# Optimization experiments

Measured on AMD Instinct MI355X. Metric: run time of the kernel, lower is better.

## Reference

```python
import jax, jax.numpy as jnp
import numpy as np

K = 3  # number of SGC propagation hops


def setup_inputs() -> dict:
    key = jax.random.key(0)
    k1, k2, k3 = jax.random.split(key, 3)
    N, E, F = 50000, 800000, 128
    x = jax.random.normal(k1, (N, F), dtype=jnp.float32)
    edge_index = jax.random.randint(k2, (2, E), 0, N, dtype=jnp.int64)
    weight = jax.random.normal(k3, (F, 1), dtype=jnp.float32) * (1.0 / np.sqrt(F))
    bias = jnp.zeros((1,), dtype=jnp.float32)
    return {"x": x, "edge_index": edge_index, "weight": weight, "bias": bias}


def reference(x, edge_index, weight, bias):
    N = x.shape[0]
    # gcn_norm: add self-loops, symmetric normalization D^-1/2 (A+I) D^-1/2
    loops = jnp.arange(N, dtype=edge_index.dtype)
    src = jnp.concatenate([edge_index[0], loops])  # message sources
    dst = jnp.concatenate([edge_index[1], loops])  # aggregation targets
    ones = jnp.ones(src.shape[0], dtype=x.dtype)
    deg = jax.ops.segment_sum(ones, dst, num_segments=N)  # [N]
    dinv = jnp.where(deg > 0, jax.lax.rsqrt(deg), 0.0)
    norm = (dinv[src] * dinv[dst])[:, None]  # [E+N, 1]
    # K hops of S @ x
    for _ in range(K):
        x = jax.ops.segment_sum(norm * x[src], dst, num_segments=N)
    out = x @ weight + bias  # [N, 1]
    return jnp.square(out)
```

## Files before the change

kernel.cpp:

```cpp
#include <hip/hip_runtime.h>

#define FEAT 128
#define NPB 98
#define SBITS 25
#define SMASK ((1u << SBITS) - 1u)
#define NSCAT 256
#define CAPB 32
#define CAPB_SHIFT 5
#define CAP2 4096
#define CAP2_SHIFT 12
#define NGEMV 256
#define TPB 256
#define LINE 32
#define NBHIST 512

__device__ __forceinline__ void astore_f(float* p, float v) {
    __hip_atomic_store(p, v, __ATOMIC_RELAXED, __HIP_MEMORY_SCOPE_AGENT);
}
__device__ __forceinline__ void astore_i(int* p, int v) {
    __hip_atomic_store(p, v, __ATOMIC_RELAXED, __HIP_MEMORY_SCOPE_AGENT);
}
__device__ __forceinline__ int aload_i(const int* p) {
    return __hip_atomic_load(p, __ATOMIC_RELAXED, __HIP_MEMORY_SCOPE_AGENT);
}

__device__ __forceinline__ void wbar(int* arr, int* flags, int b, int ep) {
    __syncthreads();
    if (threadIdx.x == 0) {
        astore_i(&arr[b], ep);
        while (aload_i(&flags[b * LINE]) < ep) __builtin_amdgcn_s_sleep(1);
    }
    __syncthreads();
}

__global__ void k1_scat_gemv(const float* __restrict__ x, const int* __restrict__ src,
                             const int* __restrict__ dst, const float* __restrict__ w,
                             int N, int E, int NB, int chunk,
                             unsigned* __restrict__ ebuf, unsigned char* __restrict__ cnt2,
                             float* __restrict__ z) {
    const int b = blockIdx.x;
    const int t = threadIdx.x;
    if (b < NSCAT) {
        __shared__ int h[NBHIST];
        for (int i = t; i < NB; i += TPB) h[i] = 0;
        __syncthreads();
        int beg = b * chunk;
        int end = min(E, beg + chunk);
        for (int e = beg + t; e < end; e += TPB) {
            int s = src[e], d = dst[e];
            int bk  = (int)((unsigned)d / NPB);
            int loc = d - bk * NPB;
            int l = atomicAdd(&h[bk], 1);
            if (l < CAPB)
                ebuf[((size_t)(bk * NSCAT + b) << CAPB_SHIFT) + l] =
                    ((unsigned)loc << SBITS) | (unsigned)s;
        }
        __syncthreads();
        for (int i = t; i < NB; i += TPB)
            cnt2[(size_t)i * NSCAT + b] = (unsigned char)min(h[i], CAPB);
    } else {
        int gb  = b - NSCAT;
        int hw  = t >> 5;
        int l32 = t & 31;
        float4 wv = ((const float4*)w)[l32];
        for (int node = gb * 8 + hw; node < N; node += NGEMV * 8) {
            float4 xv = ((const float4*)(x + (size_t)node * FEAT))[l32];
            float s = xv.x * wv.x + xv.y * wv.y + xv.z * wv.z + xv.w * wv.w;
            #pragma unroll
            for (int o = 16; o >= 1; o >>= 1) s += __shfl_xor(s, o, 64);
            if (l32 == 0) z[node] = s;
        }
    }
}

__global__ void __launch_bounds__(TPB, 2) k2_fused(
    const unsigned* __restrict__ ebuf, const unsigned char* __restrict__ cnt2,
    const float* __restrict__ z, const float* __restrict__ bias,
    unsigned* __restrict__ ebuf2,
    float* __restrict__ u0, float* __restrict__ u1, float* __restrict__ u2,
    float* __restrict__ out, int* __restrict__ arr, int* __restrict__ flags,
    int N, int NB)
{
    const int b = blockIdx.x;
    const int t = threadIdx.x;

    if (b == NB) {
        for (int ep = 1; ep <= 3; ++ep) {
            for (;;) {
                int ok = 1;
                for (int i = t; i < NB; i += TPB)
                    if (aload_i(&arr[i]) < ep) { ok = 0; break; }
                if (__syncthreads_and(ok)) break;
                __builtin_amdgcn_s_sleep(2);
            }
            for (int i = t; i < NB; i += TPB)
                astore_i(&flags[i * LINE], ep);
        }
        return;
    }

    __shared__ float uown[NPB], dinvL[NPB], acc[NPB];
    __shared__ int   degL[NPB];
    __shared__ int   pref[TPB];
    __shared__ int   cntB_s;
    const int base = b * NPB;
    const int nn   = min(NPB, N - base);

    if (t < NPB) degL[t] = 0;
    __syncthreads();
    int cnt = cnt2[(size_t)b * NSCAT + t];
    pref[t] = cnt;
    __syncthreads();
    #pragma unroll
    for (int off = 1; off < TPB; off <<= 1) {
        int v = (t >= off) ? pref[t - off] : 0;
        __syncthreads();
        pref[t] += v;
        __syncthreads();
    }
    int mypos = pref[t] - cnt;
    if (t == TPB - 1) cntB_s = min(pref[t], CAP2);
    {
        const unsigned* cell = ebuf + ((size_t)(b * NSCAT + t) << CAPB_SHIFT);
        unsigned* dst2 = ebuf2 + ((size_t)b << CAP2_SHIFT);
        #pragma unroll 4
        for (int j = 0; j < cnt; ++j) {
            unsigned p = cell[j];
            atomicAdd(&degL[p >> SBITS], 1);
            int pos = mypos + j;
            if (pos < CAP2) dst2[pos] = p;
        }
    }
    __syncthreads();
    if (t < nn) {
        float dv = 1.0f / sqrtf(1.0f + (float)degL[t]);
        dinvL[t] = dv;
        float u = dv * z[base + t];
        uown[t] = u;
        astore_f(&u0[base + t], u);
    }
    wbar(arr, flags, b, 1);

    const unsigned* dst2 = ebuf2 + ((size_t)b << CAP2_SHIFT);
    const int cntB = cntB_s;

    if (t < NPB) acc[t] = 0.0f;
    __syncthreads();
    for (int j = t; j < cntB; j += TPB) {
        unsigned p = dst2[j];
        atomicAdd(&acc[p >> SBITS], u0[p & SMASK]);
    }
    __syncthreads();
    if (t < nn) {
        float dv = dinvL[t];
        float nu = dv * dv * (acc[t] + uown[t]);
        uown[t] = nu;
        astore_f(&u1[base + t], nu);
    }
    wbar(arr, flags, b, 2);

    if (t < NPB) acc[t] = 0.0f;
    __syncthreads();
    for (int j = t; j < cntB; j += TPB) {
        unsigned p = dst2[j];
        atomicAdd(&acc[p >> SBITS], u1[p & SMASK]);
    }
    __syncthreads();
    if (t < nn) {
        float dv = dinvL[t];
        float nu = dv * dv * (acc[t] + uown[t]);
        uown[t] = nu;
        astore_f(&u2[base + t], nu);
    }
    wbar(arr, flags, b, 3);

    if (t < NPB) acc[t] = 0.0f;
    __syncthreads();
    for (int j = t; j < cntB; j += TPB) {
        unsigned p = dst2[j];
        atomicAdd(&acc[p >> SBITS], u2[p & SMASK]);
    }
    __syncthreads();
    if (t < nn) {
        float dv = dinvL[t];
        float v = dv * (acc[t] + uown[t]) + bias[0];
        out[base + t] = v * v;
    }
    if (t == 0) { astore_i(&arr[b], 0); astore_i(&flags[b * LINE], 0); }
}

__global__ void f_init_deg(float* __restrict__ deg, int N) {
    int i = blockIdx.x * blockDim.x + threadIdx.x;
    if (i < N) deg[i] = 1.0f;
}
__global__ void f_count_deg(const int* __restrict__ dst, float* __restrict__ deg, int E) {
    int e = blockIdx.x * blockDim.x + threadIdx.x;
    if (e < E) unsafeAtomicAdd(&deg[dst[e]], 1.0f);
}
__global__ void f_dot_dinv(const float* __restrict__ x, const float* __restrict__ w,
                           const float* __restrict__ deg, float* __restrict__ dinv,
                           float* __restrict__ z, int N) {
    int wid  = (blockIdx.x * blockDim.x + threadIdx.x) >> 6;
    int lane = threadIdx.x & 63;
    if (wid >= N) return;
    const float2* xr = reinterpret_cast<const float2*>(x + (size_t)wid * FEAT);
    const float2* wr = reinterpret_cast<const float2*>(w);
    float2 xv = xr[lane];
    float2 wv = wr[lane];
    float s = xv.x * wv.x + xv.y * wv.y;
    #pragma unroll
    for (int o = 32; o >= 1; o >>= 1) s += __shfl_xor(s, o, 64);
    if (lane == 0) { z[wid] = s; dinv[wid] = 1.0f / sqrtf(deg[wid]); }
}
__global__ void f_hop_self(const float* __restrict__ za, const float* __restrict__ dinv,
                           float* __restrict__ zb, int N) {
    int i = blockIdx.x * blockDim.x + threadIdx.x;
    if (i < N) { float d = dinv[i]; zb[i] = d * d * za[i]; }
}
__global__ void f_hop_edges(const int* __restrict__ src, const int* __restrict__ dst,
                            const float* __restrict__ za, const float* __restrict__ dinv,
                            float* __restrict__ zb, int E) {
    int e = blockIdx.x * blockDim.x + threadIdx.x;
    if (e < E) {
        int s = src[e], d = dst[e];
        unsafeAtomicAdd(&zb[d], dinv[s] * dinv[d] * za[s]);
    }
}
__global__ void f_final(const float* __restrict__ z, const float* __restrict__ bias,
                        float* __restrict__ out, int N) {
    int i = blockIdx.x * blockDim.x + threadIdx.x;
    if (i < N) { float v = z[i] + bias[0]; out[i] = v * v; }
}

extern "C" void kernel_launch(void* const* d_in, const int* in_sizes, int n_in,
                              void* d_out, int out_size, void* d_ws, size_t ws_size,
                              hipStream_t stream) {
    const float* x    = (const float*)d_in[0];
    const int*   ei   = (const int*)d_in[1];
    const float* w    = (const float*)d_in[2];
    const float* bias = (const float*)d_in[3];
    float*       out  = (float*)d_out;

    const int N = in_sizes[0] / FEAT;
    const int E = in_sizes[1] / 2;
    const int* src = ei;
    const int* dst = ei + E;

    const int NB = (N + NPB - 1) / NPB;

    size_t ebuf_b  = (size_t)NB * NSCAT * CAPB * sizeof(unsigned);
    size_t ebuf2_b = (size_t)NB * CAP2 * sizeof(unsigned);
    size_t off_e2    = ebuf_b;
    size_t off_z     = off_e2 + ebuf2_b;
    size_t off_arr   = (off_z + (size_t)4 * N * sizeof(float) + 255) & ~(size_t)255;
    size_t off_flags = (off_arr + (size_t)NB * sizeof(int) + 255) & ~(size_t)255;
    size_t off_cnt2  = off_flags + (size_t)NB * LINE * sizeof(int);
    size_t need      = off_cnt2 + (size_t)NB * NSCAT + 256;

    bool fast = (NB + 1 <= 512) && (N <= (1 << SBITS)) &&
                ((size_t)E <= (size_t)8 * NB * NSCAT) &&
                ((size_t)E * 2 <= (size_t)NB * CAP2) &&
                (ws_size >= need);

    if (fast) {
        unsigned*      ebuf  = (unsigned*)d_ws;
        unsigned*      ebuf2 = (unsigned*)((char*)d_ws + off_e2);
        float*         z     = (float*)((char*)d_ws + off_z);
        float*         u0    = z + N;
        float*         u1    = u0 + N;
        float*         u2    = u1 + N;
        int*           arr   = (int*)((char*)d_ws + off_arr);
        int*           flags = (int*)((char*)d_ws + off_flags);
        unsigned char* cnt2  = (unsigned char*)((char*)d_ws + off_cnt2);

        const int chunk = (E + NSCAT - 1) / NSCAT;

        k1_scat_gemv<<<NSCAT + NGEMV, TPB, 0, stream>>>(x, src, dst, w, N, E, NB,
                                                        chunk, ebuf, cnt2, z);
        k2_fused<<<NB + 1, TPB, 0, stream>>>(ebuf, cnt2, z, bias, ebuf2,
                                             u0, u1, u2, out, arr, flags, N, NB);
    } else {
        float* deg  = (float*)d_ws;
        float* dinv = deg;
        float* z0   = deg + N;
        float* z1   = z0 + N;
        const int B = 256;
        const int gN = (N + B - 1) / B;
        const int gE = (E + B - 1) / B;
        const int gW = (N * 64 + B - 1) / B;
        f_init_deg<<<gN, B, 0, stream>>>(deg, N);
        f_count_deg<<<gE, B, 0, stream>>>(dst, deg, E);
        f_dot_dinv<<<gW, B, 0, stream>>>(x, w, deg, dinv, z0, N);
        f_hop_self<<<gN, B, 0, stream>>>(z0, dinv, z1, N);
        f_hop_edges<<<gE, B, 0, stream>>>(src, dst, z0, dinv, z1, E);
        f_hop_self<<<gN, B, 0, stream>>>(z1, dinv, z0, N);
        f_hop_edges<<<gE, B, 0, stream>>>(src, dst, z1, dinv, z0, E);
        f_hop_self<<<gN, B, 0, stream>>>(z0, dinv, z1, N);
        f_hop_edges<<<gE, B, 0, stream>>>(src, dst, z0, dinv, z1, E);
        f_final<<<gN, B, 0, stream>>>(z1, bias, out, N);
    }
}
```

Measured before the change: 53.24 us.

## Replace coordinator-block grid barrier with hierarchical group-counter barrier

Removes the dedicated coordinator block that polled every block's arrival and released per-block flags. Instead, blocks atomically increment a per-group counter; the last arriver of each group of 16 sets a group flag, and all blocks poll the small set of group flags. The counters are reset in the first kernel instead of at the end of the second. The edge-aggregation loops also read four packed edges at once with a uint4 load. The intent is to cut barrier latency and serial polling; the cost is every block polling all group flags and the uint4 loads relying on buffer alignment and padding.

```diff
diff --git a/kernel.cpp b/kernel.cpp
--- a/kernel.cpp
+++ b/kernel.cpp
@@ -12,6 +12,8 @@
 #define NGEMV 256
 #define TPB 256
 #define LINE 32
+#define GSH 4
+#define GS (1 << GSH)
 #define NBHIST 512
 
 __device__ __forceinline__ void astore_f(float* p, float v) {
@@ -24,23 +26,37 @@
     return __hip_atomic_load(p, __ATOMIC_RELAXED, __HIP_MEMORY_SCOPE_AGENT);
 }
 
-__device__ __forceinline__ void wbar(int* arr, int* flags, int b, int ep) {
+__device__ __forceinline__ void gbar(int* gcnt, int* gflag, int nb, int ngrp, int ep) {
     __syncthreads();
     if (threadIdx.x == 0) {
-        astore_i(&arr[b], ep);
-        while (aload_i(&flags[b * LINE]) < ep) __builtin_amdgcn_s_sleep(1);
-    }
-    __syncthreads();
+        int g = blockIdx.x >> GSH;
+        int gsize = min(GS, nb - (g << GSH));
+        int old = __hip_atomic_fetch_add(&gcnt[g * LINE], 1,
+                                         __ATOMIC_RELAXED, __HIP_MEMORY_SCOPE_AGENT);
+        if (old == ep * gsize - 1)
+            astore_i(&gflag[g * LINE], ep);
+    }
+    for (;;) {
+        int ok = 1;
+        if (threadIdx.x < ngrp)
+            ok = (aload_i(&gflag[threadIdx.x * LINE]) >= ep);
+        if (__syncthreads_and(ok)) break;
+        __builtin_amdgcn_s_sleep(2);
+    }
 }
 
 __global__ void k1_scat_gemv(const float* __restrict__ x, const int* __restrict__ src,
                              const int* __restrict__ dst, const float* __restrict__ w,
-                             int N, int E, int NB, int chunk,
+                             int N, int E, int NB, int NGRP, int chunk,
                              unsigned* __restrict__ ebuf, unsigned char* __restrict__ cnt2,
-                             float* __restrict__ z) {
+                             float* __restrict__ z, int* __restrict__ gcnt,
+                             int* __restrict__ gflag) {
     const int b = blockIdx.x;
     const int t = threadIdx.x;
     if (b < NSCAT) {
+        if (b == 0 && t < LINE * 2) {
+            if (t < NGRP) { gcnt[t * LINE] = 0; gflag[t * LINE] = 0; }
+        }
         __shared__ int h[NBHIST];
         for (int i = t; i < NB; i += TPB) h[i] = 0;
         __syncthreads();
@@ -78,26 +94,11 @@
     const float* __restrict__ z, const float* __restrict__ bias,
     unsigned* __restrict__ ebuf2,
     float* __restrict__ u0, float* __restrict__ u1, float* __restrict__ u2,
-    float* __restrict__ out, int* __restrict__ arr, int* __restrict__ flags,
-    int N, int NB)
+    float* __restrict__ out, int* __restrict__ gcnt, int* __restrict__ gflag,
+    int N, int NB, int NGRP)
 {
     const int b = blockIdx.x;
     const int t = threadIdx.x;
-
-    if (b == NB) {
-        for (int ep = 1; ep <= 3; ++ep) {
-            for (;;) {
-                int ok = 1;
-                for (int i = t; i < NB; i += TPB)
-                    if (aload_i(&arr[i]) < ep) { ok = 0; break; }
-                if (__syncthreads_and(ok)) break;
-                __builtin_amdgcn_s_sleep(2);
-            }
-            for (int i = t; i < NB; i += TPB)
-                astore_i(&flags[i * LINE], ep);
-        }
-        return;
-    }
 
     __shared__ float uown[NPB], dinvL[NPB], acc[NPB];
     __shared__ int   degL[NPB];
@@ -139,16 +140,19 @@
         uown[t] = u;
         astore_f(&u0[base + t], u);
     }
-    wbar(arr, flags, b, 1);
+    gbar(gcnt, gflag, NB, NGRP, 1);
 
     const unsigned* dst2 = ebuf2 + ((size_t)b << CAP2_SHIFT);
     const int cntB = cntB_s;
 
     if (t < NPB) acc[t] = 0.0f;
     __syncthreads();
-    for (int j = t; j < cntB; j += TPB) {
-        unsigned p = dst2[j];
-        atomicAdd(&acc[p >> SBITS], u0[p & SMASK]);
+    for (int j = t * 4; j < cntB; j += TPB * 4) {
+        uint4 q = *(const uint4*)(dst2 + j);
+        atomicAdd(&acc[q.x >> SBITS], u0[q.x & SMASK]);
+        if (j + 1 < cntB) atomicAdd(&acc[q.y >> SBITS], u0[q.y & SMASK]);
+        if (j + 2 < cntB) atomicAdd(&acc[q.z >> SBITS], u0[q.z & SMASK]);
+        if (j + 3 < cntB) atomicAdd(&acc[q.w >> SBITS], u0[q.w & SMASK]);
     }
     __syncthreads();
     if (t < nn) {
@@ -157,13 +161,16 @@
         uown[t] = nu;
         astore_f(&u1[base + t], nu);
     }
-    wbar(arr, flags, b, 2);
+    gbar(gcnt, gflag, NB, NGRP, 2);
 
     if (t < NPB) acc[t] = 0.0f;
     __syncthreads();
-    for (int j = t; j < cntB; j += TPB) {
-        unsigned p = dst2[j];
-        atomicAdd(&acc[p >> SBITS], u1[p & SMASK]);
+    for (int j = t * 4; j < cntB; j += TPB * 4) {
+        uint4 q = *(const uint4*)(dst2 + j);
+        atomicAdd(&acc[q.x >> SBITS], u1[q.x & SMASK]);
+        if (j + 1 < cntB) atomicAdd(&acc[q.y >> SBITS], u1[q.y & SMASK]);
+        if (j + 2 < cntB) atomicAdd(&acc[q.z >> SBITS], u1[q.z & SMASK]);
+        if (j + 3 < cntB) atomicAdd(&acc[q.w >> SBITS], u1[q.w & SMASK]);
     }
     __syncthreads();
     if (t < nn) {
@@ -172,13 +179,16 @@
         uown[t] = nu;
         astore_f(&u2[base + t], nu);
     }
-    wbar(arr, flags, b, 3);
+    gbar(gcnt, gflag, NB, NGRP, 3);
 
     if (t < NPB) acc[t] = 0.0f;
     __syncthreads();
-    for (int j = t; j < cntB; j += TPB) {
-        unsigned p = dst2[j];
-        atomicAdd(&acc[p >> SBITS], u2[p & SMASK]);
+    for (int j = t * 4; j < cntB; j += TPB * 4) {
+        uint4 q = *(const uint4*)(dst2 + j);
+        atomicAdd(&acc[q.x >> SBITS], u2[q.x & SMASK]);
+        if (j + 1 < cntB) atomicAdd(&acc[q.y >> SBITS], u2[q.y & SMASK]);
+        if (j + 2 < cntB) atomicAdd(&acc[q.z >> SBITS], u2[q.z & SMASK]);
+        if (j + 3 < cntB) atomicAdd(&acc[q.w >> SBITS], u2[q.w & SMASK]);
     }
     __syncthreads();
     if (t < nn) {
@@ -186,7 +196,6 @@
         float v = dv * (acc[t] + uown[t]) + bias[0];
         out[base + t] = v * v;
     }
-    if (t == 0) { astore_i(&arr[b], 0); astore_i(&flags[b * LINE], 0); }
 }
 
 __global__ void f_init_deg(float* __restrict__ deg, int N) {
@@ -246,18 +255,19 @@
     const int* src = ei;
     const int* dst = ei + E;
 
-    const int NB = (N + NPB - 1) / NPB;
+    const int NB   = (N + NPB - 1) / NPB;
+    const int NGRP = (NB + GS - 1) >> GSH;
 
     size_t ebuf_b  = (size_t)NB * NSCAT * CAPB * sizeof(unsigned);
     size_t ebuf2_b = (size_t)NB * CAP2 * sizeof(unsigned);
     size_t off_e2    = ebuf_b;
     size_t off_z     = off_e2 + ebuf2_b;
-    size_t off_arr   = (off_z + (size_t)4 * N * sizeof(float) + 255) & ~(size_t)255;
-    size_t off_flags = (off_arr + (size_t)NB * sizeof(int) + 255) & ~(size_t)255;
-    size_t off_cnt2  = off_flags + (size_t)NB * LINE * sizeof(int);
+    size_t off_gcnt  = (off_z + (size_t)4 * N * sizeof(float) + 255) & ~(size_t)255;
+    size_t off_gflag = off_gcnt + (size_t)NGRP * LINE * sizeof(int);
+    size_t off_cnt2  = off_gflag + (size_t)NGRP * LINE * sizeof(int);
     size_t need      = off_cnt2 + (size_t)NB * NSCAT + 256;
 
-    bool fast = (NB + 1 <= 512) && (N <= (1 << SBITS)) &&
+    bool fast = (NB <= 512) && (NGRP <= LINE * 2) && (N <= (1 << SBITS)) &&
                 ((size_t)E <= (size_t)8 * NB * NSCAT) &&
                 ((size_t)E * 2 <= (size_t)NB * CAP2) &&
                 (ws_size >= need);
@@ -269,16 +279,17 @@
         float*         u0    = z + N;
         float*         u1    = u0 + N;
         float*         u2    = u1 + N;
-        int*           arr   = (int*)((char*)d_ws + off_arr);
-        int*           flags = (int*)((char*)d_ws + off_flags);
+        int*           gcnt  = (int*)((char*)d_ws + off_gcnt);
+        int*           gflag = (int*)((char*)d_ws + off_gflag);
         unsigned char* cnt2  = (unsigned char*)((char*)d_ws + off_cnt2);
 
         const int chunk = (E + NSCAT - 1) / NSCAT;
 
-        k1_scat_gemv<<<NSCAT + NGEMV, TPB, 0, stream>>>(x, src, dst, w, N, E, NB,
-                                                        chunk, ebuf, cnt2, z);
-        k2_fused<<<NB + 1, TPB, 0, stream>>>(ebuf, cnt2, z, bias, ebuf2,
-                                             u0, u1, u2, out, arr, flags, N, NB);
+        k1_scat_gemv<<<NSCAT + NGEMV, TPB, 0, stream>>>(x, src, dst, w, N, E, NB, NGRP,
+                                                        chunk, ebuf, cnt2, z,
+                                                        gcnt, gflag);
+        k2_fused<<<NB, TPB, 0, stream>>>(ebuf, cnt2, z, bias, ebuf2,
+                                         u0, u1, u2, out, gcnt, gflag, N, NB, NGRP);
     } else {
         float* deg  = (float*)d_ws;
         float* dinv = deg;
```

After: 51.31 us. 1.04x faster.
